# Kernel tuning notes

Measured on AMD Instinct MI355X. Metric: run time of the kernel, lower is better.

## Reference

```python
import jax, jax.numpy as jnp
import numpy as np


def setup_inputs() -> dict:
    key = jax.random.key(0)
    k1, k2, k3 = jax.random.split(key, 3)
    B, IN, EXP, K = 1024, 1024, 40, 7
    OUT = IN * EXP  # 40960
    x = jax.random.normal(k1, (B, IN), dtype=jnp.float32)
    # fixed fan-in projection matrix: K nonzeros per output row
    vals = jax.random.uniform(k2, (OUT, K), dtype=jnp.float32)
    idx = jax.random.randint(k3, (OUT, K), 0, IN, dtype=jnp.int32)
    return {"x": x, "vals": vals, "idx": idx}


def reference(x, vals, idx):
    # y[b, o] = sum_k vals[o, k] * x[b, idx[o, k]]
    # equivalent to (W_sparse @ x.T).T with W in COO, fixed fan-in K.
    # Loop over the small fixed fan-in K (=7) to avoid a [B, OUT, K] intermediate.
    K = idx.shape[1]
    y = x[:, idx[:, 0]] * vals[:, 0][None, :]  # [B, OUT]
    for k in range(1, K):
        y = y + x[:, idx[:, k]] * vals[:, k][None, :]
    return y
```

## Files before the change

kernel.cpp:

```cpp
#include <hip/hip_runtime.h>
#include <hip/hip_fp16.h>

#define BATCH   1024
#define IN      1024
#define OUT     40960
#define KF      7
#define BT      8
#define NO      4
#define THREADS 256
#define OTILE   (THREADS * NO)

__device__ __forceinline__ float half2_bits(__half2 h) {
    union { __half2 h; float f; } u; u.h = h; return u.f;
}

__global__ __launch_bounds__(THREADS, 4)
void sparse_proj(const float* __restrict__ x, const float* __restrict__ vals,
                 const int* __restrict__ idx, float* __restrict__ y)
{
    __shared__ __align__(16) __half xs[IN * BT];

    const int t     = threadIdx.x;
    const int b0    = blockIdx.y * BT;
    const int obase = blockIdx.x * OTILE + t;

    {
        const float* xb = x + (size_t)b0 * IN;
#pragma unroll
        for (int j = 0; j < 4; ++j) {
            const int i = t + j * THREADS;
            __half2 p0, p1, p2, p3;
            p0.x = __float2half_rn(xb[0 * IN + i]);
            p0.y = __float2half_rn(xb[1 * IN + i]);
            p1.x = __float2half_rn(xb[2 * IN + i]);
            p1.y = __float2half_rn(xb[3 * IN + i]);
            p2.x = __float2half_rn(xb[4 * IN + i]);
            p2.y = __float2half_rn(xb[5 * IN + i]);
            p3.x = __float2half_rn(xb[6 * IN + i]);
            p3.y = __float2half_rn(xb[7 * IN + i]);
            float4 f;
            f.x = half2_bits(p0);
            f.y = half2_bits(p1);
            f.z = half2_bits(p2);
            f.w = half2_bits(p3);
            *(float4*)&xs[i * 8] = f;
        }
    }
    __syncthreads();

    float acc[NO][BT];
#pragma unroll
    for (int no = 0; no < NO; ++no)
#pragma unroll
        for (int r = 0; r < BT; ++r) acc[no][r] = 0.0f;

#pragma unroll
    for (int no = 0; no < NO; ++no) {
        const int o = obase + no * THREADS;
        const int*   ip = idx  + (size_t)o * KF;
        const float* vp = vals + (size_t)o * KF;
#pragma unroll
        for (int k = 0; k < KF; ++k) {
            const int   i = ip[k];
            const float v = vp[k];
            const float4 g = *(const float4*)&xs[i * 8];
            const __half2 h0 = *(const __half2*)&g.x;
            const __half2 h1 = *(const __half2*)&g.y;
            const __half2 h2 = *(const __half2*)&g.z;
            const __half2 h3 = *(const __half2*)&g.w;
            acc[no][0] = fmaf(v, __low2float(h0),  acc[no][0]);
            acc[no][1] = fmaf(v, __high2float(h0), acc[no][1]);
            acc[no][2] = fmaf(v, __low2float(h1),  acc[no][2]);
            acc[no][3] = fmaf(v, __high2float(h1), acc[no][3]);
            acc[no][4] = fmaf(v, __low2float(h2),  acc[no][4]);
            acc[no][5] = fmaf(v, __high2float(h2), acc[no][5]);
            acc[no][6] = fmaf(v, __low2float(h3),  acc[no][6]);
            acc[no][7] = fmaf(v, __high2float(h3), acc[no][7]);
        }
    }

#pragma unroll
    for (int r = 0; r < BT; ++r) {
        float* yr = y + (size_t)(b0 + r) * OUT;
#pragma unroll
        for (int no = 0; no < NO; ++no) {
            __builtin_nontemporal_store(acc[no][r], &yr[obase + no * THREADS]);
        }
    }
}

extern "C" void kernel_launch(void* const* d_in, const int* in_sizes, int n_in,
                              void* d_out, int out_size, void* d_ws, size_t ws_size,
                              hipStream_t stream) {
    const float* x    = (const float*)d_in[0];
    const float* vals = (const float*)d_in[1];
    const int*   idx  = (const int*)d_in[2];
    float*       y    = (float*)d_out;

    dim3 grid(OUT / OTILE, BATCH / BT);
    sparse_proj<<<grid, dim3(THREADS), 0, stream>>>(x, vals, idx, y);
}
```

Before: 188.1 us.

## Add repack kernel for coalesced idx/vals and pre-packed fp16 x tiles

Adds a prologue kernel that converts x to fp16 once, interleaved 8 rows per column, and transposes idx/vals into per-64-lane chunks with k-major order. idx is stored as 16-bit byte offsets. The main kernel then loads coalesced idx/vals, where before each lane read a strided row of 7. It also fills shared memory with plain float4 copies instead of converting x once per block. The cost is an extra launch and a workspace round trip for the repacked data.

```diff
diff --git a/kernel.cpp b/kernel.cpp
--- a/kernel.cpp
+++ b/kernel.cpp
@@ -9,14 +9,43 @@
 #define NO      4
 #define THREADS 256
 #define OTILE   (THREADS * NO)
+#define CHUNKS  (OUT / 64)
 
-__device__ __forceinline__ float half2_bits(__half2 h) {
-    union { __half2 h; float f; } u; u.h = h; return u.f;
+#define PV_BYTES  ((size_t)CHUNKS * KF * 64 * 4)
+#define XPK_BYTES ((size_t)(BATCH / 8) * IN * 8 * 2)
+#define PIDX_BYTES ((size_t)CHUNKS * KF * 64 * 2)
+
+
+__global__ __launch_bounds__(THREADS)
+void repack_kernel(const float* __restrict__ x, const float* __restrict__ vals,
+                   const int* __restrict__ idx,
+                   float* __restrict__ pvals, __half* __restrict__ xpk,
+                   unsigned short* __restrict__ pidx)
+{
+    const int gid = blockIdx.x * THREADS + threadIdx.x;
+    if (blockIdx.x < 512) {
+        const int g = gid >> 10;
+        const int i = gid & 1023;
+        const float* xb = x + (size_t)g * 8 * IN + i;
+        union { __half h[8]; float4 f; } u;
+#pragma unroll
+        for (int r = 0; r < 8; ++r) u.h[r] = __float2half_rn(xb[(size_t)r * IN]);
+        *(float4*)&xpk[(size_t)gid * 8] = u.f;
+    } else {
+        const int t2 = gid - 512 * THREADS;
+        const int c  = t2 / (KF * 64);
+        const int r  = t2 % (KF * 64);
+        const int k  = r >> 6;
+        const int l  = r & 63;
+        const size_t src = (size_t)(c * 64 + l) * KF + k;
+        pvals[t2] = vals[src];
+        pidx[t2]  = (unsigned short)(idx[src] << 4);
+    }
 }
 
 __global__ __launch_bounds__(THREADS, 4)
-void sparse_proj(const float* __restrict__ x, const float* __restrict__ vals,
-                 const int* __restrict__ idx, float* __restrict__ y)
+void sparse_proj(const float* __restrict__ pvals, const __half* __restrict__ xpk,
+                 const unsigned short* __restrict__ pidx, float* __restrict__ y)
 {
     __shared__ __align__(16) __half xs[IN * BT];
 
@@ -25,26 +54,10 @@
     const int obase = blockIdx.x * OTILE + t;
 
     {
-        const float* xb = x + (size_t)b0 * IN;
+        const float4* src = (const float4*)(xpk + (size_t)blockIdx.y * IN * 8);
+        float4* dst = (float4*)xs;
 #pragma unroll
-        for (int j = 0; j < 4; ++j) {
-            const int i = t + j * THREADS;
-            __half2 p0, p1, p2, p3;
-            p0.x = __float2half_rn(xb[0 * IN + i]);
-            p0.y = __float2half_rn(xb[1 * IN + i]);
-            p1.x = __float2half_rn(xb[2 * IN + i]);
-            p1.y = __float2half_rn(xb[3 * IN + i]);
-            p2.x = __float2half_rn(xb[4 * IN + i]);
-            p2.y = __float2half_rn(xb[5 * IN + i]);
-            p3.x = __float2half_rn(xb[6 * IN + i]);
-            p3.y = __float2half_rn(xb[7 * IN + i]);
-            float4 f;
-            f.x = half2_bits(p0);
-            f.y = half2_bits(p1);
-            f.z = half2_bits(p2);
-            f.w = half2_bits(p3);
-            *(float4*)&xs[i * 8] = f;
-        }
+        for (int r = 0; r < 4; ++r) dst[t + r * THREADS] = src[t + r * THREADS];
     }
     __syncthreads();
 
@@ -54,16 +67,19 @@
 #pragma unroll
         for (int r = 0; r < BT; ++r) acc[no][r] = 0.0f;
 
+    const int w    = t >> 6;
+    const int lane = t & 63;
+
 #pragma unroll
     for (int no = 0; no < NO; ++no) {
-        const int o = obase + no * THREADS;
-        const int*   ip = idx  + (size_t)o * KF;
-        const float* vp = vals + (size_t)o * KF;
+        const int c = blockIdx.x * 16 + no * 4 + w;
+        const unsigned short* ipp = pidx  + (size_t)c * (KF * 64) + lane;
+        const float*          vpp = pvals + (size_t)c * (KF * 64) + lane;
 #pragma unroll
         for (int k = 0; k < KF; ++k) {
-            const int   i = ip[k];
-            const float v = vp[k];
-            const float4 g = *(const float4*)&xs[i * 8];
+            const unsigned off = ipp[k * 64];
+            const float v      = vpp[k * 64];
+            const float4 g = *(const float4*)((const char*)xs + off);
             const __half2 h0 = *(const __half2*)&g.x;
             const __half2 h1 = *(const __half2*)&g.y;
             const __half2 h2 = *(const __half2*)&g.z;
@@ -97,6 +113,13 @@
     const int*   idx  = (const int*)d_in[2];
     float*       y    = (float*)d_out;
 
+    float*          pvals = (float*)d_ws;
+    __half*         xpk   = (__half*)((char*)d_ws + PV_BYTES);
+    unsigned short* pidx  = (unsigned short*)((char*)d_ws + PV_BYTES + XPK_BYTES);
+
+    repack_kernel<<<dim3(512 + 1120), dim3(THREADS), 0, stream>>>(
+        x, vals, idx, pvals, xpk, pidx);
+
     dim3 grid(OUT / OTILE, BATCH / BT);
-    sparse_proj<<<grid, dim3(THREADS), 0, stream>>>(x, vals, idx, y);
+    sparse_proj<<<grid, dim3(THREADS), 0, stream>>>(pvals, xpk, pidx, y);
 }
```

Measured after the change: 177.4 us. -5.7%, faster.
